# Performance work log

Measured on AMD Instinct MI355X. Metric: run time of the kernel, lower is better.

The kernel has to match this reference:

```python
import jax, jax.numpy as jnp
import numpy as np
from itertools import combinations

B, F, C, MAX_ORDER = 4096, 32, 128, 3


def setup_inputs() -> dict:
    key = jax.random.key(0)
    ks = jax.random.split(key, 1 + MAX_ORDER)
    x = jax.random.normal(ks[0], (B, F), dtype=jnp.float32)
    # Exact combinatorial index lists, matching get_index_lists (all k-subsets, lexicographic)
    idx = [jnp.asarray(np.array(list(combinations(range(F), o)), dtype=np.int32))
           for o in range(1, MAX_ORDER + 1)]
    # Per-order Dense kernels [n_combos, num_classes] (glorot-ish scale), no bias (use_bias=False)
    Ws = [jax.random.normal(ks[i + 1], (idx[i].shape[0], C), dtype=jnp.float32)
          * (2.0 / (idx[i].shape[0] + C)) ** 0.5 for i in range(MAX_ORDER)]
    bias = jnp.zeros((1, C), dtype=jnp.float32)  # Zeros initializer
    return {"x": x, "bias": bias,
            "W1": Ws[0], "W2": Ws[1], "W3": Ws[2],
            "idx1": idx[0], "idx2": idx[1], "idx3": idx[2]}


def reference(x, bias, W1, W2, W3, idx1, idx2, idx3):
    # combine(): out = tile(bias) + sum_i Dense_i( prod over feature-subset of order i )
    out = jnp.broadcast_to(bias, (x.shape[0], bias.shape[1]))
    for idx, W in ((idx1, W1), (idx2, W2), (idx3, W3)):
        # x[:, idx]: [B, n_combos, order] gather; product over subset axis -> [B, n_combos]
        prods = jnp.prod(x[:, idx], axis=2)
        out = out + prods @ W  # [B, num_classes]
    return out
```

## Files before the change

kernel.cpp:

```cpp
#include <hip/hip_runtime.h>
#include <hip/hip_bf16.h>

constexpr int B_   = 4096;
constexpr int C_   = 128;
constexpr int K1   = 32;
constexpr int K2   = 496;
constexpr int K3   = 4960;
constexpr int KTOT = K1 + K2 + K3;
constexpr int KPAD = 5632;

constexpr int NCHUNK = KPAD / 16;
constexpr int NQ     = 4;
constexpr int QCH    = NCHUNK / NQ;

typedef __attribute__((ext_vector_type(8)))  short bf16x8;
typedef __attribute__((ext_vector_type(16))) float f32x16;

constexpr size_t WS_WT   = 0;
constexpr size_t WS_PART = 2ull << 20;

struct Sched { short a[KPAD]; short b[KPAD]; short c[KPAD]; };
constexpr Sched make_sched() {
    Sched s{}; int k = 0;
    for (int i = 0; i < 32; ++i) { s.a[k] = i; s.b[k] = 32; s.c[k] = 32; ++k; }
    for (int i = 0; i < 32; ++i)
        for (int j = i + 1; j < 32; ++j) { s.a[k] = i; s.b[k] = j; s.c[k] = 32; ++k; }
    for (int i = 0; i < 32; ++i)
        for (int j = i + 1; j < 32; ++j)
            for (int l = j + 1; l < 32; ++l) { s.a[k] = i; s.b[k] = j; s.c[k] = l; ++k; }
    for (; k < KPAD; ++k) { s.a[k] = 32; s.b[k] = 32; s.c[k] = 32; }
    return s;
}
constexpr Sched SCH = make_sched();

template<int K>
__device__ __forceinline__ float prodK(const float (&xv)[33]) {
    return xv[SCH.a[K]] * xv[SCH.b[K]] * xv[SCH.c[K]];
}

template<int K0, int J>
__device__ __forceinline__ void prods8(const float (&xv)[33], bool hi, float (&q)[8]) {
    if constexpr (J < 8) {
        q[J] = hi ? prodK<K0 + 8 + J>(xv) : prodK<K0 + J>(xv);
        prods8<K0, J + 1>(xv, hi, q);
    }
}

template<int Q, int CH>
__device__ __forceinline__ void run_chunks(const float (&xv)[33], bool hi, int lane, int ct,
                                           const ushort* __restrict__ Wb, f32x16& acc) {
    if constexpr (CH < QCH) {
        constexpr int G  = Q * QCH + CH;
        constexpr int K0 = G * 16;
        bf16x8 b0 = *(const bf16x8*)(Wb + ((size_t)(G * 4 + ct) * 64 + lane) * 8);
        float q[8];
        prods8<K0, 0>(xv, hi, q);
        union { ushort us[8]; bf16x8 v; } af;
        #pragma unroll
        for (int j = 0; j < 8; ++j) {
            __hip_bfloat16 h = __float2bfloat16(q[j]);
            af.us[j] = *reinterpret_cast<ushort*>(&h);
        }
        acc = __builtin_amdgcn_mfma_f32_32x32x16_bf16(af.v, b0, acc, 0, 0, 0);
        run_chunks<Q, CH + 1>(xv, hi, lane, ct, Wb, acc);
    }
}

__global__ __launch_bounds__(256)
void prep_wt(const float* __restrict__ W1,
             const float* __restrict__ W2,
             const float* __restrict__ W3,
             ushort* __restrict__ Wb)
{
    __shared__ ushort tile[16 * 130];
    const int gc = blockIdx.x, t = threadIdx.x;
    const int k0 = gc * 16;
    #pragma unroll
    for (int p = 0; p < 2; ++p) {
        int e  = p * 256 + t;
        int kk = e >> 5, cq = e & 31;
        int k  = k0 + kk;
        float4 v = {0.f, 0.f, 0.f, 0.f};
        if (k < K1)           v = ((const float4*)W1)[k * 32 + cq];
        else if (k < K1 + K2) v = ((const float4*)W2)[(k - K1) * 32 + cq];
        else if (k < KTOT)    v = ((const float4*)W3)[(k - K1 - K2) * 32 + cq];
        union { ushort u[4]; uint2 d; } o;
        __hip_bfloat16 h0 = __float2bfloat16(v.x); o.u[0] = *(ushort*)&h0;
        __hip_bfloat16 h1 = __float2bfloat16(v.y); o.u[1] = *(ushort*)&h1;
        __hip_bfloat16 h2 = __float2bfloat16(v.z); o.u[2] = *(ushort*)&h2;
        __hip_bfloat16 h3 = __float2bfloat16(v.w); o.u[3] = *(ushort*)&h3;
        *(uint2*)&tile[kk * 130 + cq * 4] = o.d;
    }
    __syncthreads();
    {
        int ct = t >> 6, lane = t & 63, n = lane & 31, kg = lane >> 5;
        union { ushort us[8]; uint4 d; } o;
        #pragma unroll
        for (int j = 0; j < 8; ++j) o.us[j] = tile[(kg * 8 + j) * 130 + ct * 32 + n];
        *(uint4*)&Wb[((size_t)(gc * 4 + ct) * 64 + lane) * 8] = o.d;
    }
}

__global__ __launch_bounds__(256, 2)
void poly_mfma(const float* __restrict__ x,
               const ushort* __restrict__ Wb,
               float* __restrict__ part)
{
    const int t    = threadIdx.x;
    const int lane = t & 63;
    const int w    = t >> 6;
    const int m    = lane & 31;
    const bool hi  = lane >= 32;
    const int row0 = blockIdx.x * 32;

    float xv[33];
    {
        const float4* xrow = (const float4*)(x + (size_t)(row0 + m) * 32);
        #pragma unroll
        for (int qv = 0; qv < 8; ++qv) {
            float4 v = xrow[qv];
            xv[qv * 4 + 0] = v.x; xv[qv * 4 + 1] = v.y;
            xv[qv * 4 + 2] = v.z; xv[qv * 4 + 3] = v.w;
        }
        xv[32] = 1.0f;
    }

    f32x16 acc;
    #pragma unroll
    for (int i = 0; i < 16; ++i) acc[i] = 0.f;

    switch (blockIdx.y) {
        case 0:  run_chunks<0, 0>(xv, hi, lane, w, Wb, acc); break;
        case 1:  run_chunks<1, 0>(xv, hi, lane, w, Wb, acc); break;
        case 2:  run_chunks<2, 0>(xv, hi, lane, w, Wb, acc); break;
        default: run_chunks<3, 0>(xv, hi, lane, w, Wb, acc); break;
    }

    const int kg = hi ? 1 : 0;
    float* base = part + (((size_t)blockIdx.y * B_ + row0) * C_ + w * 32);
    #pragma unroll
    for (int e = 0; e < 16; ++e) {
        int r = (e & 3) + 8 * (e >> 2) + 4 * kg;
        base[(size_t)r * C_ + m] = acc[e];
    }
}

__global__ __launch_bounds__(256)
void reduce_out(const float* __restrict__ part,
                const float* __restrict__ bias,
                float* __restrict__ out)
{
    const int idx = blockIdx.x * 256 + threadIdx.x;
    const int r   = idx >> 5;
    const int c   = (idx & 31) * 4;
    float4 s = *(const float4*)&bias[c];
    #pragma unroll
    for (int y = 0; y < NQ; ++y) {
        float4 v = *(const float4*)&part[((size_t)y * B_ + r) * C_ + c];
        s.x += v.x; s.y += v.y; s.z += v.z; s.w += v.w;
    }
    *(float4*)&out[(size_t)r * C_ + c] = s;
}

extern "C" void kernel_launch(void* const* d_in, const int* in_sizes, int n_in,
                              void* d_out, int out_size, void* d_ws, size_t ws_size,
                              hipStream_t stream)
{
    const float* x    = (const float*)d_in[0];
    const float* bias = (const float*)d_in[1];
    const float* W1   = (const float*)d_in[2];
    const float* W2   = (const float*)d_in[3];
    const float* W3   = (const float*)d_in[4];

    float* out  = (float*)d_out;
    ushort* Wb  = (ushort*)((char*)d_ws + WS_WT);
    float*  prt = (float*)((char*)d_ws + WS_PART);

    prep_wt<<<NCHUNK, 256, 0, stream>>>(W1, W2, W3, Wb);

    dim3 grid(B_ / 32, NQ);
    poly_mfma<<<grid, 256, 0, stream>>>(x, Wb, prt);

    reduce_out<<<(B_ * C_ / 4) / 256, 256, 0, stream>>>(prt, bias, out);
}
```

Before: 89.14 us.

## Split product generation into separate kernel and run bf16 GEMM on materialized features

Replaces the fused kernel, which built the triple-product features inside the MFMA loop, with a separate prodgen kernel that writes all bf16 products to a global buffer of about 46 MB. A standalone GEMM kernel then streams A and B tiles with 8-deep loads, two accumulators and a 2-way K split. The aim is to remove the per-chunk ALU product and convert work that stalled the matrix pipeline. In exchange it adds a large global write and reread of the product matrix and one more kernel launch.

```diff
diff --git a/kernel.cpp b/kernel.cpp
--- a/kernel.cpp
+++ b/kernel.cpp
@@ -10,60 +10,37 @@
 constexpr int KPAD = 5632;
 
 constexpr int NCHUNK = KPAD / 16;
-constexpr int NQ     = 4;
-constexpr int QCH    = NCHUNK / NQ;
 
 typedef __attribute__((ext_vector_type(8)))  short bf16x8;
 typedef __attribute__((ext_vector_type(16))) float f32x16;
 
 constexpr size_t WS_WT   = 0;
-constexpr size_t WS_PART = 2ull << 20;
-
-struct Sched { short a[KPAD]; short b[KPAD]; short c[KPAD]; };
-constexpr Sched make_sched() {
-    Sched s{}; int k = 0;
-    for (int i = 0; i < 32; ++i) { s.a[k] = i; s.b[k] = 32; s.c[k] = 32; ++k; }
+constexpr size_t WS_P    = 2ull << 20;
+constexpr size_t WS_PART = 64ull << 20;
+
+struct alignas(16) PKTab { unsigned v[KPAD]; };
+constexpr PKTab make_pk() {
+    PKTab t{}; int k = 0;
+    for (int i = 0; i < 32; ++i) t.v[k++] = (unsigned)i | (32u << 6) | (32u << 12);
     for (int i = 0; i < 32; ++i)
-        for (int j = i + 1; j < 32; ++j) { s.a[k] = i; s.b[k] = j; s.c[k] = 32; ++k; }
+        for (int j = i + 1; j < 32; ++j) t.v[k++] = (unsigned)i | ((unsigned)j << 6) | (32u << 12);
     for (int i = 0; i < 32; ++i)
         for (int j = i + 1; j < 32; ++j)
-            for (int l = j + 1; l < 32; ++l) { s.a[k] = i; s.b[k] = j; s.c[k] = l; ++k; }
-    for (; k < KPAD; ++k) { s.a[k] = 32; s.b[k] = 32; s.c[k] = 32; }
-    return s;
-}
-constexpr Sched SCH = make_sched();
-
-template<int K>
-__device__ __forceinline__ float prodK(const float (&xv)[33]) {
-    return xv[SCH.a[K]] * xv[SCH.b[K]] * xv[SCH.c[K]];
-}
-
-template<int K0, int J>
-__device__ __forceinline__ void prods8(const float (&xv)[33], bool hi, float (&q)[8]) {
-    if constexpr (J < 8) {
-        q[J] = hi ? prodK<K0 + 8 + J>(xv) : prodK<K0 + J>(xv);
-        prods8<K0, J + 1>(xv, hi, q);
-    }
-}
-
-template<int Q, int CH>
-__device__ __forceinline__ void run_chunks(const float (&xv)[33], bool hi, int lane, int ct,
-                                           const ushort* __restrict__ Wb, f32x16& acc) {
-    if constexpr (CH < QCH) {
-        constexpr int G  = Q * QCH + CH;
-        constexpr int K0 = G * 16;
-        bf16x8 b0 = *(const bf16x8*)(Wb + ((size_t)(G * 4 + ct) * 64 + lane) * 8);
-        float q[8];
-        prods8<K0, 0>(xv, hi, q);
-        union { ushort us[8]; bf16x8 v; } af;
-        #pragma unroll
-        for (int j = 0; j < 8; ++j) {
-            __hip_bfloat16 h = __float2bfloat16(q[j]);
-            af.us[j] = *reinterpret_cast<ushort*>(&h);
-        }
-        acc = __builtin_amdgcn_mfma_f32_32x32x16_bf16(af.v, b0, acc, 0, 0, 0);
-        run_chunks<Q, CH + 1>(xv, hi, lane, ct, Wb, acc);
-    }
+            for (int l = j + 1; l < 32; ++l)
+                t.v[k++] = (unsigned)i | ((unsigned)j << 6) | ((unsigned)l << 12);
+    for (; k < KPAD; ++k) t.v[k] = 32u | (32u << 6) | (32u << 12);
+    return t;
+}
+constexpr PKTab PKg = make_pk();
+
+__device__ __forceinline__ unsigned cvt_pk_bf16(float lo, float hi) {
+    unsigned r;
+    asm("v_cvt_pk_bf16_f32 %0, %1, %2" : "=v"(r) : "v"(lo), "v"(hi));
+    return r;
+}
+
+__device__ __forceinline__ bf16x8 ldb(const ushort* __restrict__ Wb, int G4ct, int lane) {
+    return *(const bf16x8*)(Wb + ((size_t)G4ct * 64 + lane) * 8);
 }
 
 __global__ __launch_bounds__(256)
@@ -101,47 +78,96 @@
     }
 }
 
-__global__ __launch_bounds__(256, 2)
-void poly_mfma(const float* __restrict__ x,
+__global__ __launch_bounds__(256)
+void prodgen(const float* __restrict__ x, ushort* __restrict__ P)
+{
+    __shared__ float xt[33 * 20];
+    const int t  = threadIdx.x;
+    const int r0 = blockIdx.x * 16;
+
+    #pragma unroll
+    for (int p = 0; p < 2; ++p) {
+        int e = p * 256 + t;
+        int r = e >> 5, c = e & 31;
+        xt[c * 20 + r] = x[(size_t)(r0 + r) * 32 + c];
+    }
+    if (t < 16) xt[32 * 20 + t] = 1.0f;
+    __syncthreads();
+
+    #pragma unroll 1
+    for (int it = 0; it < 11; ++it) {
+        int K2 = it * 256 + t;
+        uint2 pk = *(const uint2*)&PKg.v[K2 * 2];
+        int a0i = pk.x & 63, b0i = (pk.x >> 6) & 63, c0i = (pk.x >> 12) & 63;
+        int a1i = pk.y & 63, b1i = (pk.y >> 6) & 63, c1i = (pk.y >> 12) & 63;
+        float p0[16], p1[16];
+        #pragma unroll
+        for (int rg = 0; rg < 4; ++rg) {
+            float4 xa0 = *(const float4*)&xt[a0i * 20 + rg * 4];
+            float4 xb0 = *(const float4*)&xt[b0i * 20 + rg * 4];
+            float4 xc0 = *(const float4*)&xt[c0i * 20 + rg * 4];
+            float4 xa1 = *(const float4*)&xt[a1i * 20 + rg * 4];
+            float4 xb1 = *(const float4*)&xt[b1i * 20 + rg * 4];
+            float4 xc1 = *(const float4*)&xt[c1i * 20 + rg * 4];
+            p0[rg * 4 + 0] = xa0.x * xb0.x * xc0.x;
+            p0[rg * 4 + 1] = xa0.y * xb0.y * xc0.y;
+            p0[rg * 4 + 2] = xa0.z * xb0.z * xc0.z;
+            p0[rg * 4 + 3] = xa0.w * xb0.w * xc0.w;
+            p1[rg * 4 + 0] = xa1.x * xb1.x * xc1.x;
+            p1[rg * 4 + 1] = xa1.y * xb1.y * xc1.y;
+            p1[rg * 4 + 2] = xa1.z * xb1.z * xc1.z;
+            p1[rg * 4 + 3] = xa1.w * xb1.w * xc1.w;
+        }
+        #pragma unroll
+        for (int r = 0; r < 16; ++r) {
+            unsigned d = cvt_pk_bf16(p0[r], p1[r]);
+            *(unsigned*)&P[(size_t)(r0 + r) * KPAD + (size_t)K2 * 2] = d;
+        }
+    }
+}
+
+__global__ __launch_bounds__(64)
+void poly_gemm(const ushort* __restrict__ P,
                const ushort* __restrict__ Wb,
                float* __restrict__ part)
 {
-    const int t    = threadIdx.x;
-    const int lane = t & 63;
-    const int w    = t >> 6;
-    const int m    = lane & 31;
-    const bool hi  = lane >= 32;
-    const int row0 = blockIdx.x * 32;
-
-    float xv[33];
-    {
-        const float4* xrow = (const float4*)(x + (size_t)(row0 + m) * 32);
-        #pragma unroll
-        for (int qv = 0; qv < 8; ++qv) {
-            float4 v = xrow[qv];
-            xv[qv * 4 + 0] = v.x; xv[qv * 4 + 1] = v.y;
-            xv[qv * 4 + 2] = v.z; xv[qv * 4 + 3] = v.w;
-        }
-        xv[32] = 1.0f;
-    }
-
-    f32x16 acc;
-    #pragma unroll
-    for (int i = 0; i < 16; ++i) acc[i] = 0.f;
-
-    switch (blockIdx.y) {
-        case 0:  run_chunks<0, 0>(xv, hi, lane, w, Wb, acc); break;
-        case 1:  run_chunks<1, 0>(xv, hi, lane, w, Wb, acc); break;
-        case 2:  run_chunks<2, 0>(xv, hi, lane, w, Wb, acc); break;
-        default: run_chunks<3, 0>(xv, hi, lane, w, Wb, acc); break;
-    }
-
-    const int kg = hi ? 1 : 0;
-    float* base = part + (((size_t)blockIdx.y * B_ + row0) * C_ + w * 32);
+    const int bid   = blockIdx.x;
+    const int R     = (bid & 7) | ((bid >> 6) << 3);
+    const int inner = (bid >> 3) & 7;
+    const int ct    = inner >> 1;
+    const int kh    = inner & 1;
+    const int lane  = threadIdx.x;
+    const int m     = lane & 31;
+    const int kg    = lane >> 5;
+
+    const ushort* Arow = P + (size_t)(R * 32 + m) * KPAD + kg * 8;
+    const int c0 = kh * (NCHUNK / 2);
+
+    f32x16 a0, a1;
+    #pragma unroll
+    for (int i = 0; i < 16; ++i) { a0[i] = 0.f; a1[i] = 0.f; }
+
+    #pragma unroll 1
+    for (int g = 0; g < 22; ++g) {
+        const int kc = c0 + g * 8;
+        bf16x8 A[8], Bv[8];
+        #pragma unroll
+        for (int u = 0; u < 8; ++u) {
+            A[u]  = *(const bf16x8*)(Arow + (size_t)(kc + u) * 16);
+            Bv[u] = ldb(Wb, (kc + u) * 4 + ct, lane);
+        }
+        #pragma unroll
+        for (int u = 0; u < 8; ++u) {
+            if (u & 1) a1 = __builtin_amdgcn_mfma_f32_32x32x16_bf16(A[u], Bv[u], a1, 0, 0, 0);
+            else       a0 = __builtin_amdgcn_mfma_f32_32x32x16_bf16(A[u], Bv[u], a0, 0, 0, 0);
+        }
+    }
+
+    float* base = part + ((size_t)kh * B_ + R * 32) * C_ + ct * 32;
     #pragma unroll
     for (int e = 0; e < 16; ++e) {
         int r = (e & 3) + 8 * (e >> 2) + 4 * kg;
-        base[(size_t)r * C_ + m] = acc[e];
+        base[(size_t)r * C_ + m] = a0[e] + a1[e];
     }
 }
 
@@ -155,7 +181,7 @@
     const int c   = (idx & 31) * 4;
     float4 s = *(const float4*)&bias[c];
     #pragma unroll
-    for (int y = 0; y < NQ; ++y) {
+    for (int y = 0; y < 2; ++y) {
         float4 v = *(const float4*)&part[((size_t)y * B_ + r) * C_ + c];
         s.x += v.x; s.y += v.y; s.z += v.z; s.w += v.w;
     }
@@ -171,15 +197,14 @@
     const float* W1   = (const float*)d_in[2];
     const float* W2   = (const float*)d_in[3];
     const float* W3   = (const float*)d_in[4];
-
-    float* out  = (float*)d_out;
+    float* out = (float*)d_out;
+
     ushort* Wb  = (ushort*)((char*)d_ws + WS_WT);
+    ushort* P   = (ushort*)((char*)d_ws + WS_P);
     float*  prt = (float*)((char*)d_ws + WS_PART);
 
     prep_wt<<<NCHUNK, 256, 0, stream>>>(W1, W2, W3, Wb);
-
-    dim3 grid(B_ / 32, NQ);
-    poly_mfma<<<grid, 256, 0, stream>>>(x, Wb, prt);
-
+    prodgen<<<B_ / 16, 256, 0, stream>>>(x, P);
+    poly_gemm<<<1024, 64, 0, stream>>>(P, Wb, prt);
     reduce_out<<<(B_ * C_ / 4) / 256, 256, 0, stream>>>(prt, bias, out);
 }
```

Result: slower. 136.7 us (+53.4%).
